# Kernel tuning notes

Hardware: AMD Instinct MI355X
Metric: run time of the kernel (lower is better)

The kernel has to match this reference:

```python
import jax, jax.numpy as jnp
import numpy as np

N_NODES = 50000
N_EDGES = 800000
NODE_DIM = 128
EDGE_DIM = 64
HIDDEN = 128
OUT_DIM = 64


def graph_conv(x, W, b, src, dst, num_segments):
    # h = linear(x); out[dst] += h[src]  (scatter-add / segment-sum aggregation)
    h = x @ W + b
    return jax.ops.segment_sum(h[src], dst, num_segments=num_segments)


def setup_inputs() -> dict:
    key = jax.random.key(0)
    ks = jax.random.split(key, 12)
    s = 1.0 / np.sqrt(HIDDEN)
    return {
        "node_features": jax.random.normal(ks[0], (N_NODES, NODE_DIM), dtype=jnp.float32),
        "edge_index": jax.random.randint(ks[1], (2, N_EDGES), 0, N_NODES, dtype=jnp.int64),
        "edge_features": jax.random.normal(ks[2], (N_EDGES, EDGE_DIM), dtype=jnp.float32),
        "edge_meta_index": jax.random.randint(ks[3], (2, N_EDGES), 0, N_EDGES, dtype=jnp.int64),
        "W1": jax.random.normal(ks[4], (NODE_DIM, HIDDEN), dtype=jnp.float32) * s,
        "b1": jnp.zeros((HIDDEN,), dtype=jnp.float32),
        "W2": jax.random.normal(ks[5], (HIDDEN, HIDDEN), dtype=jnp.float32) * s,
        "b2": jnp.zeros((HIDDEN,), dtype=jnp.float32),
        "We": jax.random.normal(ks[6], (EDGE_DIM, HIDDEN), dtype=jnp.float32) * s,
        "be": jnp.zeros((HIDDEN,), dtype=jnp.float32),
        "Wfc": jax.random.normal(ks[7], (2 * HIDDEN, OUT_DIM), dtype=jnp.float32) * s,
        "bfc": jnp.zeros((OUT_DIM,), dtype=jnp.float32),
    }


def reference(node_features, edge_index, edge_features, edge_meta_index,
              W1, b1, W2, b2, We, be, Wfc, bfc):
    row, col = edge_index[0], edge_index[1]
    mrow, mcol = edge_meta_index[0], edge_meta_index[1]

    # two node GraphConvs (dropout is identity in eval / p=0)
    x = jax.nn.relu(graph_conv(node_features, W1, b1, row, col, N_NODES))
    x = jax.nn.relu(graph_conv(x, W2, b2, row, col, N_NODES))

    # edge GraphConv on the line graph: e has one row per original edge
    e = graph_conv(edge_features, We, be, mrow, mcol, N_EDGES)

    # per-edge scatter-add aggregation (vectorized form of the Python loop):
    # aggregated_neighbors[dest] += x[src]; aggregated_edges[dest] += e[idx]
    agg_neighbors = jax.ops.segment_sum(x[row], col, num_segments=N_NODES)
    agg_edges = jax.ops.segment_sum(e, col, num_segments=N_NODES)

    out = jnp.concatenate([x + agg_neighbors, agg_edges], axis=1) @ Wfc + bfc
    return out
```

## Files before the change

kernel.cpp:

```cpp
#include <hip/hip_runtime.h>

#define N_NODES 50000
#define N_EDGES 800000
#define NODE_DIM 128
#define EDGE_DIM 64
#define HIDDEN 128
#define OUT_DIM 64

#define NBKT 196
#define CAP 4864
#define EPB 4096
#define NBLK1 196

typedef unsigned short u16;
typedef unsigned int u32;
typedef __attribute__((ext_vector_type(8))) short bf16x8;
typedef __attribute__((ext_vector_type(4))) float f32x4;

__device__ __forceinline__ float bflo(u32 u) { return __builtin_bit_cast(float, u << 16); }
__device__ __forceinline__ float bfhi(u32 u) { return __builtin_bit_cast(float, u & 0xFFFF0000u); }
__device__ __forceinline__ u32 pack2(float x, float y) {
    u32 a = __builtin_bit_cast(u32, x);
    a += 0x7FFFu + ((a >> 16) & 1u);
    u32 b = __builtin_bit_cast(u32, y);
    b += 0x7FFFu + ((b >> 16) & 1u);
    return (a >> 16) | (b & 0xFFFF0000u);
}
__device__ __forceinline__ u16 bf16r(float x) {
    u32 a = __builtin_bit_cast(u32, x);
    a += 0x7FFFu + ((a >> 16) & 1u);
    return (u16)(a >> 16);
}

__global__ __launch_bounds__(256) void pre1(
    const float* __restrict__ We, const float* __restrict__ be,
    const float* __restrict__ Wfc, const float* __restrict__ W1,
    const float* __restrict__ W2,
    float* __restrict__ Wcomb, float* __restrict__ bvec,
    short* __restrict__ W1t, short* __restrict__ W2t,
    int* __restrict__ bcur, int* __restrict__ bcurm)
{
    int idx = blockIdx.x * 256 + threadIdx.x;
    if (idx < 4096) {
        int k = idx >> 6, c = idx & 63;
        float s = 0.f;
        for (int h = 0; h < 128; h++)
            s = fmaf(We[k * 128 + h], Wfc[(128 + h) * 64 + c], s);
        Wcomb[idx] = s;
    } else if (idx < 4160) {
        int c = idx - 4096;
        float s = 0.f;
        for (int h = 0; h < 128; h++)
            s = fmaf(be[h], Wfc[(128 + h) * 64 + c], s);
        bvec[c] = s;
    } else if (idx < 20544) {
        int i = idx - 4160; int n = i >> 7, k = i & 127;
        W1t[n * 128 + k] = (short)bf16r(W1[k * 128 + n]);
    } else if (idx < 36928) {
        int i = idx - 20544; int n = i >> 7, k = i & 127;
        W2t[n * 128 + k] = (short)bf16r(W2[k * 128 + n]);
    } else if (idx < 37320) {
        int i = idx - 36928;
        if (i < 196) bcur[i] = i * CAP;
        else bcurm[i - 196] = (i - 196) * CAP;
    }
}

__global__ __launch_bounds__(256) void pre2(
    const float* __restrict__ Wfc, const float* __restrict__ Wcomb,
    short* __restrict__ Wft)
{
    int idx = blockIdx.x * 256 + threadIdx.x;
    if (idx < 64 * 192) {
        int n = idx / 192, k = idx - n * 192;
        float v = (k < 128) ? Wfc[k * 64 + n] : Wcomb[(k - 128) * 64 + n];
        Wft[n * 192 + k] = (short)bf16r(v);
    }
}

__global__ __launch_bounds__(256) void bin_pairs(
    const int* __restrict__ row, const int* __restrict__ col,
    const int* __restrict__ mrow, const int* __restrict__ mcol,
    int* __restrict__ bcur, int* __restrict__ bcurm,
    u32* __restrict__ pairs, u32* __restrict__ pairsm)
{
    int prob = (blockIdx.x >= NBLK1) ? 1 : 0;
    int blk = blockIdx.x - prob * NBLK1;
    int base = blk * EPB;
    int t = threadIdx.x;
    __shared__ int lh[NBKT];
    __shared__ int lbase[NBKT];
    __shared__ int lcur[NBKT];
    for (int i = t; i < NBKT; i += 256) { lh[i] = 0; lcur[i] = 0; }
    __syncthreads();
    int k[16], v[16];
    #pragma unroll
    for (int i = 0; i < 16; i++) {
        int idx = base + i * 256 + t;
        if (idx < N_EDGES) {
            if (!prob) { k[i] = col[idx]; v[i] = row[idx]; }
            else       { k[i] = col[mcol[idx]]; v[i] = mrow[idx]; }
            atomicAdd(&lh[k[i] >> 8], 1);
        } else {
            k[i] = -1; v[i] = 0;
        }
    }
    __syncthreads();
    int* gcur = prob ? bcurm : bcur;
    for (int i = t; i < NBKT; i += 256)
        lbase[i] = atomicAdd(&gcur[i], lh[i]);
    __syncthreads();
    u32* PR = prob ? pairsm : pairs;
    #pragma unroll
    for (int i = 0; i < 16; i++) {
        if (k[i] >= 0) {
            int bk = k[i] >> 8;
            int p = lbase[bk] + atomicAdd(&lcur[bk], 1);
            if (p < (bk + 1) * CAP)
                PR[p] = (u32)v[i] | ((u32)(k[i] & 255) << 24);
        }
    }
}

__global__ __launch_bounds__(256) void bucket_fill(
    const u32* __restrict__ pairs, const u32* __restrict__ pairsm,
    const int* __restrict__ bcur, const int* __restrict__ bcurm,
    int* __restrict__ offp, int* __restrict__ deg, int* __restrict__ ids,
    int* __restrict__ offpm, int* __restrict__ degm, int* __restrict__ idsm)
{
    int prob = (blockIdx.x >= NBKT) ? 1 : 0;
    int b = blockIdx.x - prob * NBKT;
    const u32* PR = prob ? pairsm : pairs;
    int cnt_total = (prob ? bcurm[b] : bcur[b]) - b * CAP;
    if (cnt_total > CAP) cnt_total = CAP;
    int n0 = b << 8;
    int nn = N_NODES - n0; if (nn > 256) nn = 256;
    __shared__ int hist[256];
    __shared__ int cur[256];
    __shared__ int wsum[4];
    __shared__ u32 pbuf[CAP];
    int t = threadIdx.x;
    hist[t] = 0;
    __syncthreads();
    for (int i = t; i < cnt_total; i += 256) {
        u32 pr = PR[(size_t)b * CAP + i];
        pbuf[i] = pr;
        atomicAdd(&hist[pr >> 24], 1);
    }
    __syncthreads();
    int h = hist[t];
    int x = h;
    int lane = t & 63, wid = t >> 6;
    for (int d = 1; d < 64; d <<= 1) {
        int u = __shfl_up(x, d, 64);
        if (lane >= d) x += u;
    }
    if (lane == 63) wsum[wid] = x;
    __syncthreads();
    int wex = 0;
    for (int i = 0; i < wid; i++) wex += wsum[i];
    int excl = wex + x - h;
    cur[t] = excl;
    if (t < nn) {
        if (!prob) { offp[n0 + t] = b * CAP + excl; deg[n0 + t] = h; }
        else       { offpm[n0 + t] = b * CAP + excl; degm[n0 + t] = h; }
    }
    __syncthreads();
    int* OI = prob ? idsm : ids;
    for (int i = t; i < cnt_total; i += 256) {
        u32 pr = pbuf[i];
        int p = atomicAdd(&cur[pr >> 24], 1);
        OI[(size_t)b * CAP + p] = (int)(pr & 0xFFFFFFu);
    }
}

__global__ __launch_bounds__(256) void gemm_mfma_f32(
    const float* __restrict__ A, const short* __restrict__ Wt,
    u16* __restrict__ P, int M)
{
    __shared__ short As[64 * 128];
    __shared__ short Ws[128 * 128];
    int t = threadIdx.x;
    int r0 = blockIdx.x * 64;
    for (int i = t; i < 64 * 32; i += 256) {
        int row = i >> 5, c4 = i & 31;
        int gr = r0 + row;
        float4 v = make_float4(0.f, 0.f, 0.f, 0.f);
        if (gr < M) v = ((const float4*)(A + (size_t)gr * 128))[c4];
        uint2 u; u.x = pack2(v.x, v.y); u.y = pack2(v.z, v.w);
        *(uint2*)((char*)As + row * 256 + ((c4 * 8) ^ ((row & 7) << 4))) = u;
    }
    for (int i = t; i < 128 * 16; i += 256) {
        int row = i >> 4, c16 = i & 15;
        uint4 u = *(const uint4*)((const char*)Wt + row * 256 + c16 * 16);
        *(uint4*)((char*)Ws + row * 256 + ((c16 * 16) ^ ((row & 7) << 4))) = u;
    }
    __syncthreads();
    int w = t >> 6, l = t & 63, lr = l & 15, q = l >> 4;
    int rh = (w & 1) * 32, ch = (w >> 1) * 64;
    f32x4 acc[2][4];
    #pragma unroll
    for (int rt = 0; rt < 2; rt++)
        #pragma unroll
        for (int ct = 0; ct < 4; ct++) acc[rt][ct] = (f32x4){0.f, 0.f, 0.f, 0.f};
    #pragma unroll
    for (int kk = 0; kk < 4; kk++) {
        int bo = kk * 64 + q * 16;
        bf16x8 a[2];
        #pragma unroll
        for (int rt = 0; rt < 2; rt++) {
            int ar = rh + rt * 16 + lr;
            a[rt] = *(const bf16x8*)((const char*)As + ar * 256 + (bo ^ ((ar & 7) << 4)));
        }
        #pragma unroll
        for (int ct = 0; ct < 4; ct++) {
            int br = ch + ct * 16 + lr;
            bf16x8 b = *(const bf16x8*)((const char*)Ws + br * 256 + (bo ^ ((br & 7) << 4)));
            acc[0][ct] = __builtin_amdgcn_mfma_f32_16x16x32_bf16(a[0], b, acc[0][ct], 0, 0, 0);
            acc[1][ct] = __builtin_amdgcn_mfma_f32_16x16x32_bf16(a[1], b, acc[1][ct], 0, 0, 0);
        }
    }
    #pragma unroll
    for (int rt = 0; rt < 2; rt++)
        #pragma unroll
        for (int reg = 0; reg < 4; reg++) {
            int gr = r0 + rh + rt * 16 + q * 4 + reg;
            if (gr < M) {
                #pragma unroll
                for (int ct = 0; ct < 4; ct++)
                    P[(size_t)gr * 128 + ch + ct * 16 + lr] = bf16r(acc[rt][ct][reg]);
            }
        }
}

__global__ __launch_bounds__(256) void gemm_mfma_bf16(
    const u16* __restrict__ A, const short* __restrict__ Wt,
    u16* __restrict__ P, int M)
{
    __shared__ short As[64 * 128];
    __shared__ short Ws[128 * 128];
    int t = threadIdx.x;
    int r0 = blockIdx.x * 64;
    for (int i = t; i < 64 * 16; i += 256) {
        int row = i >> 4, c16 = i & 15;
        int gr = r0 + row;
        uint4 u = make_uint4(0u, 0u, 0u, 0u);
        if (gr < M) u = *(const uint4*)((const char*)A + (size_t)gr * 256 + c16 * 16);
        *(uint4*)((char*)As + row * 256 + ((c16 * 16) ^ ((row & 7) << 4))) = u;
    }
    for (int i = t; i < 128 * 16; i += 256) {
        int row = i >> 4, c16 = i & 15;
        uint4 u = *(const uint4*)((const char*)Wt + row * 256 + c16 * 16);
        *(uint4*)((char*)Ws + row * 256 + ((c16 * 16) ^ ((row & 7) << 4))) = u;
    }
    __syncthreads();
    int w = t >> 6, l = t & 63, lr = l & 15, q = l >> 4;
    int rh = (w & 1) * 32, ch = (w >> 1) * 64;
    f32x4 acc[2][4];
    #pragma unroll
    for (int rt = 0; rt < 2; rt++)
        #pragma unroll
        for (int ct = 0; ct < 4; ct++) acc[rt][ct] = (f32x4){0.f, 0.f, 0.f, 0.f};
    #pragma unroll
    for (int kk = 0; kk < 4; kk++) {
        int bo = kk * 64 + q * 16;
        bf16x8 a[2];
        #pragma unroll
        for (int rt = 0; rt < 2; rt++) {
            int ar = rh + rt * 16 + lr;
            a[rt] = *(const bf16x8*)((const char*)As + ar * 256 + (bo ^ ((ar & 7) << 4)));
        }
        #pragma unroll
        for (int ct = 0; ct < 4; ct++) {
            int br = ch + ct * 16 + lr;
            bf16x8 b = *(const bf16x8*)((const char*)Ws + br * 256 + (bo ^ ((br & 7) << 4)));
            acc[0][ct] = __builtin_amdgcn_mfma_f32_16x16x32_bf16(a[0], b, acc[0][ct], 0, 0, 0);
            acc[1][ct] = __builtin_amdgcn_mfma_f32_16x16x32_bf16(a[1], b, acc[1][ct], 0, 0, 0);
        }
    }
    #pragma unroll
    for (int rt = 0; rt < 2; rt++)
        #pragma unroll
        for (int reg = 0; reg < 4; reg++) {
            int gr = r0 + rh + rt * 16 + q * 4 + reg;
            if (gr < M) {
                #pragma unroll
                for (int ct = 0; ct < 4; ct++)
                    P[(size_t)gr * 128 + ch + ct * 16 + lr] = bf16r(acc[rt][ct][reg]);
            }
        }
}

__global__ __launch_bounds__(256) void agg_relu_bf16(
    const u16* __restrict__ P, const int* __restrict__ offp,
    const int* __restrict__ deg,
    const int* __restrict__ ids, const float* __restrict__ bias,
    u16* __restrict__ X, int M)
{
    int w = blockIdx.x * 4 + (threadIdx.x >> 6);
    if (w >= M) return;
    int lane = threadIdx.x & 63;
    int q = lane >> 4;
    int l = lane & 15;
    int beg = offp[w], end = beg + deg[w];
    const uint4* F = (const uint4*)P;
    float a0 = 0.f, a1 = 0.f, a2 = 0.f, a3 = 0.f,
          a4 = 0.f, a5 = 0.f, a6 = 0.f, a7 = 0.f;
    int i = beg;
    for (; i + 7 < end; i += 8) {
        int s0 = ids[i + q], s1 = ids[i + q + 4];
        uint4 v0 = F[(size_t)s0 * 16 + l];
        uint4 v1 = F[(size_t)s1 * 16 + l];
        a0 += bflo(v0.x) + bflo(v1.x); a1 += bfhi(v0.x) + bfhi(v1.x);
        a2 += bflo(v0.y) + bflo(v1.y); a3 += bfhi(v0.y) + bfhi(v1.y);
        a4 += bflo(v0.z) + bflo(v1.z); a5 += bfhi(v0.z) + bfhi(v1.z);
        a6 += bflo(v0.w) + bflo(v1.w); a7 += bfhi(v0.w) + bfhi(v1.w);
    }
    for (int j = i + q; j < end; j += 4) {
        uint4 v = F[(size_t)ids[j] * 16 + l];
        a0 += bflo(v.x); a1 += bfhi(v.x);
        a2 += bflo(v.y); a3 += bfhi(v.y);
        a4 += bflo(v.z); a5 += bfhi(v.z);
        a6 += bflo(v.w); a7 += bfhi(v.w);
    }
    a0 += __shfl_xor(a0, 32, 64); a1 += __shfl_xor(a1, 32, 64);
    a2 += __shfl_xor(a2, 32, 64); a3 += __shfl_xor(a3, 32, 64);
    a4 += __shfl_xor(a4, 32, 64); a5 += __shfl_xor(a5, 32, 64);
    a6 += __shfl_xor(a6, 32, 64); a7 += __shfl_xor(a7, 32, 64);
    a0 += __shfl_xor(a0, 16, 64); a1 += __shfl_xor(a1, 16, 64);
    a2 += __shfl_xor(a2, 16, 64); a3 += __shfl_xor(a3, 16, 64);
    a4 += __shfl_xor(a4, 16, 64); a5 += __shfl_xor(a5, 16, 64);
    a6 += __shfl_xor(a6, 16, 64); a7 += __shfl_xor(a7, 16, 64);
    if (q == 0) {
        float dg = (float)(end - beg);
        float4 b0 = ((const float4*)bias)[2 * l];
        float4 b1 = ((const float4*)bias)[2 * l + 1];
        a0 = fmaxf(fmaf(dg, b0.x, a0), 0.f);
        a1 = fmaxf(fmaf(dg, b0.y, a1), 0.f);
        a2 = fmaxf(fmaf(dg, b0.z, a2), 0.f);
        a3 = fmaxf(fmaf(dg, b0.w, a3), 0.f);
        a4 = fmaxf(fmaf(dg, b1.x, a4), 0.f);
        a5 = fmaxf(fmaf(dg, b1.y, a5), 0.f);
        a6 = fmaxf(fmaf(dg, b1.z, a6), 0.f);
        a7 = fmaxf(fmaf(dg, b1.w, a7), 0.f);
        uint4 o;
        o.x = pack2(a0, a1); o.y = pack2(a2, a3);
        o.z = pack2(a4, a5); o.w = pack2(a6, a7);
        ((uint4*)(X + (size_t)w * 128))[l] = o;
    }
}

__global__ __launch_bounds__(256) void agg_epilogue(
    const u16* __restrict__ X2, const float* __restrict__ ef,
    const int* __restrict__ offp, const int* __restrict__ deg,
    const int* __restrict__ ids,
    const int* __restrict__ offpm, const int* __restrict__ degm,
    const int* __restrict__ mids,
    u16* __restrict__ S, u16* __restrict__ Gg, int M)
{
    int w = blockIdx.x * 4 + (threadIdx.x >> 6);
    if (w >= M) return;
    int lane = threadIdx.x & 63;
    int q = lane >> 4;
    int l = lane & 15;
    {
        int beg = offp[w], end = beg + deg[w];
        const uint4* F = (const uint4*)X2;
        float a0 = 0.f, a1 = 0.f, a2 = 0.f, a3 = 0.f,
              a4 = 0.f, a5 = 0.f, a6 = 0.f, a7 = 0.f;
        int i = beg;
        for (; i + 7 < end; i += 8) {
            int s0 = ids[i + q], s1 = ids[i + q + 4];
            uint4 v0 = F[(size_t)s0 * 16 + l];
            uint4 v1 = F[(size_t)s1 * 16 + l];
            a0 += bflo(v0.x) + bflo(v1.x); a1 += bfhi(v0.x) + bfhi(v1.x);
            a2 += bflo(v0.y) + bflo(v1.y); a3 += bfhi(v0.y) + bfhi(v1.y);
            a4 += bflo(v0.z) + bflo(v1.z); a5 += bfhi(v0.z) + bfhi(v1.z);
            a6 += bflo(v0.w) + bflo(v1.w); a7 += bfhi(v0.w) + bfhi(v1.w);
        }
        for (int j = i + q; j < end; j += 4) {
            uint4 v = F[(size_t)ids[j] * 16 + l];
            a0 += bflo(v.x); a1 += bfhi(v.x);
            a2 += bflo(v.y); a3 += bfhi(v.y);
            a4 += bflo(v.z); a5 += bfhi(v.z);
            a6 += bflo(v.w); a7 += bfhi(v.w);
        }
        a0 += __shfl_xor(a0, 32, 64); a1 += __shfl_xor(a1, 32, 64);
        a2 += __shfl_xor(a2, 32, 64); a3 += __shfl_xor(a3, 32, 64);
        a4 += __shfl_xor(a4, 32, 64); a5 += __shfl_xor(a5, 32, 64);
        a6 += __shfl_xor(a6, 32, 64); a7 += __shfl_xor(a7, 32, 64);
        a0 += __shfl_xor(a0, 16, 64); a1 += __shfl_xor(a1, 16, 64);
        a2 += __shfl_xor(a2, 16, 64); a3 += __shfl_xor(a3, 16, 64);
        a4 += __shfl_xor(a4, 16, 64); a5 += __shfl_xor(a5, 16, 64);
        a6 += __shfl_xor(a6, 16, 64); a7 += __shfl_xor(a7, 16, 64);
        if (q == 0) {
            uint4 own = F[(size_t)w * 16 + l];
            a0 += bflo(own.x); a1 += bfhi(own.x);
            a2 += bflo(own.y); a3 += bfhi(own.y);
            a4 += bflo(own.z); a5 += bfhi(own.z);
            a6 += bflo(own.w); a7 += bfhi(own.w);
            uint4 o;
            o.x = pack2(a0, a1); o.y = pack2(a2, a3);
            o.z = pack2(a4, a5); o.w = pack2(a6, a7);
            ((uint4*)(S + (size_t)w * 128))[l] = o;
        }
    }
    {
        int beg = offpm[w], end = beg + degm[w];
        const float4* E = (const float4*)ef;
        float g0 = 0.f, g1 = 0.f, g2 = 0.f, g3 = 0.f;
        int i = beg;
        for (; i + 7 < end; i += 8) {
            int s0 = mids[i + q], s1 = mids[i + q + 4];
            float4 v0 = E[(size_t)s0 * 16 + l];
            float4 v1 = E[(size_t)s1 * 16 + l];
            g0 += v0.x + v1.x; g1 += v0.y + v1.y;
            g2 += v0.z + v1.z; g3 += v0.w + v1.w;
        }
        for (int j = i + q; j < end; j += 4) {
            float4 v = E[(size_t)mids[j] * 16 + l];
            g0 += v.x; g1 += v.y; g2 += v.z; g3 += v.w;
        }
        g0 += __shfl_xor(g0, 32, 64); g1 += __shfl_xor(g1, 32, 64);
        g2 += __shfl_xor(g2, 32, 64); g3 += __shfl_xor(g3, 32, 64);
        g0 += __shfl_xor(g0, 16, 64); g1 += __shfl_xor(g1, 16, 64);
        g2 += __shfl_xor(g2, 16, 64); g3 += __shfl_xor(g3, 16, 64);
        if (q == 0) {
            uint2 o;
            o.x = pack2(g0, g1); o.y = pack2(g2, g3);
            ((uint2*)(Gg + (size_t)w * 64))[l] = o;
        }
    }
}

__global__ __launch_bounds__(256) void final_mfma(
    const u16* __restrict__ S, const u16* __restrict__ Gg,
    const int* __restrict__ degm, const short* __restrict__ Wft,
    const float* __restrict__ bvec, const float* __restrict__ bfc,
    float* __restrict__ out, int M)
{
    __shared__ short As[64 * 192];
    __shared__ short Ws[64 * 192];
    int t = threadIdx.x;
    int r0 = blockIdx.x * 64;
    for (int i = t; i < 64 * 16; i += 256) {
        int row = i >> 4, c16 = i & 15;
        int gr = r0 + row;
        uint4 u = make_uint4(0u, 0u, 0u, 0u);
        if (gr < M) u = *(const uint4*)((const char*)S + (size_t)gr * 256 + c16 * 16);
        *(uint4*)((char*)As + row * 384 + ((c16 * 16) ^ ((row & 7) << 4))) = u;
    }
    for (int i = t; i < 64 * 8; i += 256) {
        int row = i >> 3, c16 = i & 7;
        int gr = r0 + row;
        uint4 u = make_uint4(0u, 0u, 0u, 0u);
        if (gr < M) u = *(const uint4*)((const char*)Gg + (size_t)gr * 128 + c16 * 16);
        *(uint4*)((char*)As + row * 384 + ((256 + c16 * 16) ^ ((row & 7) << 4))) = u;
    }
    for (int i = t; i < 64 * 24; i += 256) {
        int row = i / 24, c16 = i - row * 24;
        uint4 u = *(const uint4*)((const char*)Wft + row * 384 + c16 * 16);
        *(uint4*)((char*)Ws + row * 384 + ((c16 * 16) ^ ((row & 7) << 4))) = u;
    }
    __syncthreads();
    int w = t >> 6, l = t & 63, lr = l & 15, q = l >> 4;
    int rh = (w & 1) * 32, ch = (w >> 1) * 32;
    f32x4 acc[2][2];
    #pragma unroll
    for (int rt = 0; rt < 2; rt++)
        #pragma unroll
        for (int ct = 0; ct < 2; ct++) acc[rt][ct] = (f32x4){0.f, 0.f, 0.f, 0.f};
    #pragma unroll
    for (int kk = 0; kk < 6; kk++) {
        int bo = kk * 64 + q * 16;
        bf16x8 a[2];
        #pragma unroll
        for (int rt = 0; rt < 2; rt++) {
            int ar = rh + rt * 16 + lr;
            a[rt] = *(const bf16x8*)((const char*)As + ar * 384 + (bo ^ ((ar & 7) << 4)));
        }
        #pragma unroll
        for (int ct = 0; ct < 2; ct++) {
            int br = ch + ct * 16 + lr;
            bf16x8 b = *(const bf16x8*)((const char*)Ws + br * 384 + (bo ^ ((br & 7) << 4)));
            acc[0][ct] = __builtin_amdgcn_mfma_f32_16x16x32_bf16(a[0], b, acc[0][ct], 0, 0, 0);
            acc[1][ct] = __builtin_amdgcn_mfma_f32_16x16x32_bf16(a[1], b, acc[1][ct], 0, 0, 0);
        }
    }
    float bv0 = bvec[ch + lr], bv1 = bvec[ch + 16 + lr];
    float bf0 = bfc[ch + lr],  bf1 = bfc[ch + 16 + lr];
    #pragma unroll
    for (int rt = 0; rt < 2; rt++)
        #pragma unroll
        for (int reg = 0; reg < 4; reg++) {
            int gr = r0 + rh + rt * 16 + q * 4 + reg;
            if (gr < M) {
                float cnt = (float)degm[gr];
                out[(size_t)gr * 64 + ch + lr]      = acc[rt][0][reg] + fmaf(cnt, bv0, bf0);
                out[(size_t)gr * 64 + ch + 16 + lr] = acc[rt][1][reg] + fmaf(cnt, bv1, bf1);
            }
        }
}

extern "C" void kernel_launch(void* const* d_in, const int* in_sizes, int n_in,
                              void* d_out, int out_size, void* d_ws, size_t ws_size,
                              hipStream_t stream)
{
    const float* nf  = (const float*)d_in[0];
    const int*   ei  = (const int*)d_in[1];
    const float* ef  = (const float*)d_in[2];
    const int*   emi = (const int*)d_in[3];
    const float* W1  = (const float*)d_in[4];
    const float* b1  = (const float*)d_in[5];
    const float* W2  = (const float*)d_in[6];
    const float* b2  = (const float*)d_in[7];
    const float* We  = (const float*)d_in[8];
    const float* be  = (const float*)d_in[9];
    const float* Wfc = (const float*)d_in[10];
    const float* bfc = (const float*)d_in[11];

    const int* row  = ei;
    const int* col  = ei + N_EDGES;
    const int* mrow = emi;
    const int* mcol = emi + N_EDGES;

    u16* A  = (u16*)d_ws;
    u16* B  = A + (size_t)N_NODES * 128;
    u16* S  = B + (size_t)N_NODES * 128;
    u16* Gg = S + (size_t)N_NODES * 128;
    u32* pairs  = (u32*)(Gg + (size_t)N_NODES * 64);
    u32* pairsm = pairs + (size_t)NBKT * CAP;
    float* Wcomb = (float*)(pairsm + (size_t)NBKT * CAP);
    float* bvec  = Wcomb + 64 * 64;
    short* W1t = (short*)(bvec + 64);
    short* W2t = W1t + 128 * 128;
    short* Wft = W2t + 128 * 128;
    int* offp  = (int*)(Wft + 64 * 192);
    int* deg   = offp + N_NODES;
    int* offpm = deg + N_NODES;
    int* degm  = offpm + N_NODES;
    int* bcur  = degm + N_NODES;
    int* bcurm = bcur + 256;
    int* ids   = bcurm + 256;
    int* idsm  = ids + (size_t)NBKT * CAP;

    pre1<<<146, 256, 0, stream>>>(We, be, Wfc, W1, W2, Wcomb, bvec, W1t, W2t, bcur, bcurm);

    bin_pairs<<<2 * NBLK1, 256, 0, stream>>>(row, col, mrow, mcol,
                                             bcur, bcurm, pairs, pairsm);
    bucket_fill<<<2 * NBKT, 256, 0, stream>>>(pairs, pairsm, bcur, bcurm,
                                              offp, deg, ids, offpm, degm, idsm);
    pre2<<<48, 256, 0, stream>>>(Wfc, Wcomb, Wft);

    gemm_mfma_f32<<<(N_NODES + 63) / 64, 256, 0, stream>>>(nf, W1t, A, N_NODES);
    agg_relu_bf16<<<(N_NODES + 3) / 4, 256, 0, stream>>>(A, offp, deg, ids, b1, B, N_NODES);
    gemm_mfma_bf16<<<(N_NODES + 63) / 64, 256, 0, stream>>>(B, W2t, A, N_NODES);
    agg_relu_bf16<<<(N_NODES + 3) / 4, 256, 0, stream>>>(A, offp, deg, ids, b2, B, N_NODES);
    agg_epilogue<<<(N_NODES + 3) / 4, 256, 0, stream>>>(
        B, ef, offp, deg, ids, offpm, degm, idsm, S, Gg, N_NODES);
    final_mfma<<<(N_NODES + 63) / 64, 256, 0, stream>>>(
        S, Gg, degm, Wft, bvec, bfc, (float*)d_out, N_NODES);
}
```

Measured before the change: 493.1 us.

## Assign one 16-lane quarter-wave per node in gather aggregation kernels

Each aggregation kernel now gives every node a 16-thread group instead of a full 64-lane wavefront, so each wave handles four nodes. The cross-lane shuffle reduction and the idle lanes during the epilogue go away, and each group walks its neighbour list with a 4-way unrolled gather. The cost is more sequential iterations per thread, about 16 per node at average degree, and load imbalance between nodes of different degree within one wave.

```diff
diff --git a/kernel.cpp b/kernel.cpp
--- a/kernel.cpp
+++ b/kernel.cpp
@@ -291,66 +291,60 @@
         }
 }
 
-__global__ __launch_bounds__(256) void agg_relu_bf16(
+__global__ __launch_bounds__(256) void agg_relu_q(
     const u16* __restrict__ P, const int* __restrict__ offp,
     const int* __restrict__ deg,
     const int* __restrict__ ids, const float* __restrict__ bias,
     u16* __restrict__ X, int M)
 {
-    int w = blockIdx.x * 4 + (threadIdx.x >> 6);
+    int qid = threadIdx.x >> 4;
+    int l = threadIdx.x & 15;
+    int w = blockIdx.x * 16 + qid;
     if (w >= M) return;
-    int lane = threadIdx.x & 63;
-    int q = lane >> 4;
-    int l = lane & 15;
     int beg = offp[w], end = beg + deg[w];
     const uint4* F = (const uint4*)P;
     float a0 = 0.f, a1 = 0.f, a2 = 0.f, a3 = 0.f,
           a4 = 0.f, a5 = 0.f, a6 = 0.f, a7 = 0.f;
     int i = beg;
-    for (; i + 7 < end; i += 8) {
-        int s0 = ids[i + q], s1 = ids[i + q + 4];
-        uint4 v0 = F[(size_t)s0 * 16 + l];
-        uint4 v1 = F[(size_t)s1 * 16 + l];
-        a0 += bflo(v0.x) + bflo(v1.x); a1 += bfhi(v0.x) + bfhi(v1.x);
-        a2 += bflo(v0.y) + bflo(v1.y); a3 += bfhi(v0.y) + bfhi(v1.y);
-        a4 += bflo(v0.z) + bflo(v1.z); a5 += bfhi(v0.z) + bfhi(v1.z);
-        a6 += bflo(v0.w) + bflo(v1.w); a7 += bfhi(v0.w) + bfhi(v1.w);
-    }
-    for (int j = i + q; j < end; j += 4) {
-        uint4 v = F[(size_t)ids[j] * 16 + l];
+    for (; i + 3 < end; i += 4) {
+        uint4 v0 = F[(size_t)ids[i]     * 16 + l];
+        uint4 v1 = F[(size_t)ids[i + 1] * 16 + l];
+        uint4 v2 = F[(size_t)ids[i + 2] * 16 + l];
+        uint4 v3 = F[(size_t)ids[i + 3] * 16 + l];
+        a0 += bflo(v0.x) + bflo(v1.x) + bflo(v2.x) + bflo(v3.x);
+        a1 += bfhi(v0.x) + bfhi(v1.x) + bfhi(v2.x) + bfhi(v3.x);
+        a2 += bflo(v0.y) + bflo(v1.y) + bflo(v2.y) + bflo(v3.y);
+        a3 += bfhi(v0.y) + bfhi(v1.y) + bfhi(v2.y) + bfhi(v3.y);
+        a4 += bflo(v0.z) + bflo(v1.z) + bflo(v2.z) + bflo(v3.z);
+        a5 += bfhi(v0.z) + bfhi(v1.z) + bfhi(v2.z) + bfhi(v3.z);
+        a6 += bflo(v0.w) + bflo(v1.w) + bflo(v2.w) + bflo(v3.w);
+        a7 += bfhi(v0.w) + bfhi(v1.w) + bfhi(v2.w) + bfhi(v3.w);
+    }
+    for (; i < end; i++) {
+        uint4 v = F[(size_t)ids[i] * 16 + l];
         a0 += bflo(v.x); a1 += bfhi(v.x);
         a2 += bflo(v.y); a3 += bfhi(v.y);
         a4 += bflo(v.z); a5 += bfhi(v.z);
         a6 += bflo(v.w); a7 += bfhi(v.w);
     }
-    a0 += __shfl_xor(a0, 32, 64); a1 += __shfl_xor(a1, 32, 64);
-    a2 += __shfl_xor(a2, 32, 64); a3 += __shfl_xor(a3, 32, 64);
-    a4 += __shfl_xor(a4, 32, 64); a5 += __shfl_xor(a5, 32, 64);
-    a6 += __shfl_xor(a6, 32, 64); a7 += __shfl_xor(a7, 32, 64);
-    a0 += __shfl_xor(a0, 16, 64); a1 += __shfl_xor(a1, 16, 64);
-    a2 += __shfl_xor(a2, 16, 64); a3 += __shfl_xor(a3, 16, 64);
-    a4 += __shfl_xor(a4, 16, 64); a5 += __shfl_xor(a5, 16, 64);
-    a6 += __shfl_xor(a6, 16, 64); a7 += __shfl_xor(a7, 16, 64);
-    if (q == 0) {
-        float dg = (float)(end - beg);
-        float4 b0 = ((const float4*)bias)[2 * l];
-        float4 b1 = ((const float4*)bias)[2 * l + 1];
-        a0 = fmaxf(fmaf(dg, b0.x, a0), 0.f);
-        a1 = fmaxf(fmaf(dg, b0.y, a1), 0.f);
-        a2 = fmaxf(fmaf(dg, b0.z, a2), 0.f);
-        a3 = fmaxf(fmaf(dg, b0.w, a3), 0.f);
-        a4 = fmaxf(fmaf(dg, b1.x, a4), 0.f);
-        a5 = fmaxf(fmaf(dg, b1.y, a5), 0.f);
-        a6 = fmaxf(fmaf(dg, b1.z, a6), 0.f);
-        a7 = fmaxf(fmaf(dg, b1.w, a7), 0.f);
-        uint4 o;
-        o.x = pack2(a0, a1); o.y = pack2(a2, a3);
-        o.z = pack2(a4, a5); o.w = pack2(a6, a7);
-        ((uint4*)(X + (size_t)w * 128))[l] = o;
-    }
-}
-
-__global__ __launch_bounds__(256) void agg_epilogue(
+    float dg = (float)(end - beg);
+    float4 b0 = ((const float4*)bias)[2 * l];
+    float4 b1 = ((const float4*)bias)[2 * l + 1];
+    a0 = fmaxf(fmaf(dg, b0.x, a0), 0.f);
+    a1 = fmaxf(fmaf(dg, b0.y, a1), 0.f);
+    a2 = fmaxf(fmaf(dg, b0.z, a2), 0.f);
+    a3 = fmaxf(fmaf(dg, b0.w, a3), 0.f);
+    a4 = fmaxf(fmaf(dg, b1.x, a4), 0.f);
+    a5 = fmaxf(fmaf(dg, b1.y, a5), 0.f);
+    a6 = fmaxf(fmaf(dg, b1.z, a6), 0.f);
+    a7 = fmaxf(fmaf(dg, b1.w, a7), 0.f);
+    uint4 o;
+    o.x = pack2(a0, a1); o.y = pack2(a2, a3);
+    o.z = pack2(a4, a5); o.w = pack2(a6, a7);
+    ((uint4*)(X + (size_t)w * 128))[l] = o;
+}
+
+__global__ __launch_bounds__(256) void agg_epilogue_q(
     const u16* __restrict__ X2, const float* __restrict__ ef,
     const int* __restrict__ offp, const int* __restrict__ deg,
     const int* __restrict__ ids,
@@ -358,78 +352,67 @@
     const int* __restrict__ mids,
     u16* __restrict__ S, u16* __restrict__ Gg, int M)
 {
-    int w = blockIdx.x * 4 + (threadIdx.x >> 6);
+    int qid = threadIdx.x >> 4;
+    int l = threadIdx.x & 15;
+    int w = blockIdx.x * 16 + qid;
     if (w >= M) return;
-    int lane = threadIdx.x & 63;
-    int q = lane >> 4;
-    int l = lane & 15;
     {
         int beg = offp[w], end = beg + deg[w];
         const uint4* F = (const uint4*)X2;
-        float a0 = 0.f, a1 = 0.f, a2 = 0.f, a3 = 0.f,
-              a4 = 0.f, a5 = 0.f, a6 = 0.f, a7 = 0.f;
+        uint4 own = F[(size_t)w * 16 + l];
+        float a0 = bflo(own.x), a1 = bfhi(own.x),
+              a2 = bflo(own.y), a3 = bfhi(own.y),
+              a4 = bflo(own.z), a5 = bfhi(own.z),
+              a6 = bflo(own.w), a7 = bfhi(own.w);
         int i = beg;
-        for (; i + 7 < end; i += 8) {
-            int s0 = ids[i + q], s1 = ids[i + q + 4];
-            uint4 v0 = F[(size_t)s0 * 16 + l];
-            uint4 v1 = F[(size_t)s1 * 16 + l];
-            a0 += bflo(v0.x) + bflo(v1.x); a1 += bfhi(v0.x) + bfhi(v1.x);
-            a2 += bflo(v0.y) + bflo(v1.y); a3 += bfhi(v0.y) + bfhi(v1.y);
-            a4 += bflo(v0.z) + bflo(v1.z); a5 += bfhi(v0.z) + bfhi(v1.z);
-            a6 += bflo(v0.w) + bflo(v1.w); a7 += bfhi(v0.w) + bfhi(v1.w);
-        }
-        for (int j = i + q; j < end; j += 4) {
-            uint4 v = F[(size_t)ids[j] * 16 + l];
+        for (; i + 3 < end; i += 4) {
+            uint4 v0 = F[(size_t)ids[i]     * 16 + l];
+            uint4 v1 = F[(size_t)ids[i + 1] * 16 + l];
+            uint4 v2 = F[(size_t)ids[i + 2] * 16 + l];
+            uint4 v3 = F[(size_t)ids[i + 3] * 16 + l];
+            a0 += bflo(v0.x) + bflo(v1.x) + bflo(v2.x) + bflo(v3.x);
+            a1 += bfhi(v0.x) + bfhi(v1.x) + bfhi(v2.x) + bfhi(v3.x);
+            a2 += bflo(v0.y) + bflo(v1.y) + bflo(v2.y) + bflo(v3.y);
+            a3 += bfhi(v0.y) + bfhi(v1.y) + bfhi(v2.y) + bfhi(v3.y);
+            a4 += bflo(v0.z) + bflo(v1.z) + bflo(v2.z) + bflo(v3.z);
+            a5 += bfhi(v0.z) + bfhi(v1.z) + bfhi(v2.z) + bfhi(v3.z);
+            a6 += bflo(v0.w) + bflo(v1.w) + bflo(v2.w) + bflo(v3.w);
+            a7 += bfhi(v0.w) + bfhi(v1.w) + bfhi(v2.w) + bfhi(v3.w);
+        }
+        for (; i < end; i++) {
+            uint4 v = F[(size_t)ids[i] * 16 + l];
             a0 += bflo(v.x); a1 += bfhi(v.x);
             a2 += bflo(v.y); a3 += bfhi(v.y);
             a4 += bflo(v.z); a5 += bfhi(v.z);
             a6 += bflo(v.w); a7 += bfhi(v.w);
         }
-        a0 += __shfl_xor(a0, 32, 64); a1 += __shfl_xor(a1, 32, 64);
-        a2 += __shfl_xor(a2, 32, 64); a3 += __shfl_xor(a3, 32, 64);
-        a4 += __shfl_xor(a4, 32, 64); a5 += __shfl_xor(a5, 32, 64);
-        a6 += __shfl_xor(a6, 32, 64); a7 += __shfl_xor(a7, 32, 64);
-        a0 += __shfl_xor(a0, 16, 64); a1 += __shfl_xor(a1, 16, 64);
-        a2 += __shfl_xor(a2, 16, 64); a3 += __shfl_xor(a3, 16, 64);
-        a4 += __shfl_xor(a4, 16, 64); a5 += __shfl_xor(a5, 16, 64);
-        a6 += __shfl_xor(a6, 16, 64); a7 += __shfl_xor(a7, 16, 64);
-        if (q == 0) {
-            uint4 own = F[(size_t)w * 16 + l];
-            a0 += bflo(own.x); a1 += bfhi(own.x);
-            a2 += bflo(own.y); a3 += bfhi(own.y);
-            a4 += bflo(own.z); a5 += bfhi(own.z);
-            a6 += bflo(own.w); a7 += bfhi(own.w);
-            uint4 o;
-            o.x = pack2(a0, a1); o.y = pack2(a2, a3);
-            o.z = pack2(a4, a5); o.w = pack2(a6, a7);
-            ((uint4*)(S + (size_t)w * 128))[l] = o;
-        }
+        uint4 o;
+        o.x = pack2(a0, a1); o.y = pack2(a2, a3);
+        o.z = pack2(a4, a5); o.w = pack2(a6, a7);
+        ((uint4*)(S + (size_t)w * 128))[l] = o;
     }
     {
         int beg = offpm[w], end = beg + degm[w];
         const float4* E = (const float4*)ef;
         float g0 = 0.f, g1 = 0.f, g2 = 0.f, g3 = 0.f;
         int i = beg;
-        for (; i + 7 < end; i += 8) {
-            int s0 = mids[i + q], s1 = mids[i + q + 4];
-            float4 v0 = E[(size_t)s0 * 16 + l];
-            float4 v1 = E[(size_t)s1 * 16 + l];
-            g0 += v0.x + v1.x; g1 += v0.y + v1.y;
-            g2 += v0.z + v1.z; g3 += v0.w + v1.w;
-        }
-        for (int j = i + q; j < end; j += 4) {
-            float4 v = E[(size_t)mids[j] * 16 + l];
+        for (; i + 3 < end; i += 4) {
+            float4 v0 = E[(size_t)mids[i]     * 16 + l];
+            float4 v1 = E[(size_t)mids[i + 1] * 16 + l];
+            float4 v2 = E[(size_t)mids[i + 2] * 16 + l];
+            float4 v3 = E[(size_t)mids[i + 3] * 16 + l];
+            g0 += v0.x + v1.x + v2.x + v3.x;
+            g1 += v0.y + v1.y + v2.y + v3.y;
+            g2 += v0.z + v1.z + v2.z + v3.z;
+            g3 += v0.w + v1.w + v2.w + v3.w;
+        }
+        for (; i < end; i++) {
+            float4 v = E[(size_t)mids[i] * 16 + l];
             g0 += v.x; g1 += v.y; g2 += v.z; g3 += v.w;
         }
-        g0 += __shfl_xor(g0, 32, 64); g1 += __shfl_xor(g1, 32, 64);
-        g2 += __shfl_xor(g2, 32, 64); g3 += __shfl_xor(g3, 32, 64);
-        g0 += __shfl_xor(g0, 16, 64); g1 += __shfl_xor(g1, 16, 64);
-        g2 += __shfl_xor(g2, 16, 64); g3 += __shfl_xor(g3, 16, 64);
-        if (q == 0) {
-            uint2 o;
-            o.x = pack2(g0, g1); o.y = pack2(g2, g3);
-            ((uint2*)(Gg + (size_t)w * 64))[l] = o;
-        }
+        uint2 o;
+        o.x = pack2(g0, g1); o.y = pack2(g2, g3);
+        ((uint2*)(Gg + (size_t)w * 64))[l] = o;
     }
 }
 
@@ -553,10 +536,10 @@
     pre2<<<48, 256, 0, stream>>>(Wfc, Wcomb, Wft);
 
     gemm_mfma_f32<<<(N_NODES + 63) / 64, 256, 0, stream>>>(nf, W1t, A, N_NODES);
-    agg_relu_bf16<<<(N_NODES + 3) / 4, 256, 0, stream>>>(A, offp, deg, ids, b1, B, N_NODES);
+    agg_relu_q<<<(N_NODES + 15) / 16, 256, 0, stream>>>(A, offp, deg, ids, b1, B, N_NODES);
     gemm_mfma_bf16<<<(N_NODES + 63) / 64, 256, 0, stream>>>(B, W2t, A, N_NODES);
-    agg_relu_bf16<<<(N_NODES + 3) / 4, 256, 0, stream>>>(A, offp, deg, ids, b2, B, N_NODES);
-    agg_epilogue<<<(N_NODES + 3) / 4, 256, 0, stream>>>(
+    agg_relu_q<<<(N_NODES + 15) / 16, 256, 0, stream>>>(A, offp, deg, ids, b2, B, N_NODES);
+    agg_epilogue_q<<<(N_NODES + 15) / 16, 256, 0, stream>>>(
         B, ef, offp, deg, ids, offpm, degm, idsm, S, Gg, N_NODES);
     final_mfma<<<(N_NODES + 63) / 64, 256, 0, stream>>>(
         S, Gg, degm, Wft, bvec, bfc, (float*)d_out, N_NODES);
```

Result: faster. 482.1 us (-2.2%).
